# Kernel tuning notes

Measured on AMD Instinct MI355X. Metric: run time of the kernel, lower is better.

Reference implementation:

```python
import jax, jax.numpy as jnp
import numpy as np

N_EXPERTS = 32
TOPK = 256
DMODEL = 1024
EXPERT_SIZE = 2048
BATCH = 2
CUTOFF = 4096


def setup_inputs() -> dict:
    key = jax.random.key(0)
    k1, k2, k3, k4 = jax.random.split(key, 4)
    x = jax.random.normal(k1, (BATCH, CUTOFF, DMODEL), dtype=jnp.float32)
    # init scales ~ 1/sqrt(fan_in), mimicking get_init_weight
    gate = jax.random.normal(k2, (CUTOFF, N_EXPERTS), dtype=jnp.float32) / np.sqrt(DMODEL)
    lin1_weight = jax.random.normal(k3, (N_EXPERTS, DMODEL, EXPERT_SIZE), dtype=jnp.float32) / np.sqrt(DMODEL)
    lin2_weight = jax.random.normal(k4, (N_EXPERTS, EXPERT_SIZE, DMODEL), dtype=jnp.float32) / np.sqrt(EXPERT_SIZE)
    return {"x": x, "gate": gate, "lin1_weight": lin1_weight, "lin2_weight": lin2_weight}


def reference(x, gate, lin1_weight, lin2_weight):
    batch_size, cutoff, dmodel = x.shape
    n_experts = lin1_weight.shape[0]
    # gate scores: (batch, cutoff, n_experts) -> (n_experts, batch*cutoff)
    gate_out = jnp.einsum('bcd,ce->bce', x, gate)
    gate_out = jnp.transpose(gate_out, (2, 0, 1)).reshape(n_experts, batch_size * cutoff)
    probs = jax.nn.softmax(gate_out, axis=1)
    # top-k token selection per expert (computed but, faithfully to the original,
    # not used to gather tokens -- the original reshapes tokens contiguously)
    topk_values, topk_indices = jax.lax.top_k(probs, TOPK)
    # contiguous token -> expert grouping (as in the original reshape)
    xe = x.reshape(n_experts, TOPK, dmodel)  # requires batch*cutoff == n_experts*topk
    h = jax.nn.relu(jnp.einsum('ekd,eds->eks', xe, lin1_weight))
    out = jnp.einsum('eks,esd->ekd', h, lin2_weight)
    return out.reshape(batch_size, cutoff, dmodel)
```

## Files before the change

### kernel.cpp

```cpp
#include <hip/hip_runtime.h>
#include <hip/hip_bf16.h>

#define NE 32
#define MM 256
#define DM 1024
#define ES 2048

typedef __attribute__((ext_vector_type(8))) short short8;
typedef __attribute__((ext_vector_type(4))) float f32x4;
typedef unsigned int uint32;
typedef unsigned long long u64;
typedef unsigned short u16;

__device__ __forceinline__ uint32 cvt_pk_bf16(float a, float b) {
    uint32 r;
    asm("v_cvt_pk_bf16_f32 %0, %1, %2" : "=v"(r) : "v"(a), "v"(b));
    return r;
}
__device__ __forceinline__ u64 pack4(float a, float b, float c, float d) {
    return (u64)cvt_pk_bf16(a, b) | ((u64)cvt_pk_bf16(c, d) << 32);
}

__device__ __forceinline__ void gl_lds16(const void* g, void* l) {
    __builtin_amdgcn_global_load_lds(
        (const __attribute__((address_space(1))) uint32*)g,
        (__attribute__((address_space(3))) uint32*)l, 16, 0, 0);
}

__device__ __forceinline__ int b_off(int n, int k) {
    int X = ((n >> 2) & 7) ^ ((n & 3) << 1);
    return n * 128 + ((((k >> 3) ^ X) & 7) << 4) + (((k >> 2) & 1) << 3);
}

__global__ __launch_bounds__(256) void cvt_bf16(const float* __restrict__ x,
                                                u16* __restrict__ xb, int n4) {
    int i = blockIdx.x * blockDim.x + threadIdx.x;
    int stride = gridDim.x * blockDim.x;
    for (; i < n4; i += stride) {
        float4 v = ((const float4*)x)[i];
        ((u64*)xb)[i] = pack4(v.x, v.y, v.z, v.w);
    }
}

template<int N, int K, bool RELU, typename CT>
__global__ __launch_bounds__(512) void ec_gemm(
    const u16* __restrict__ A,
    const float* __restrict__ B,
    CT* __restrict__ C)
{
    constexpr int BM = 256, BN = 256, BK = 64;
    constexpr int NT = N / BN;
    constexpr int NSTEP = K / BK;
    constexpr int EPX = NE / 8;

    int bid   = blockIdx.x;
    int xcd   = bid & 7;
    int local = bid >> 3;
    int e     = xcd * EPX + local / NT;
    int nt    = local % NT;

    const u16*   Ae = A + (size_t)e * MM * K;
    const float* Be = B + (size_t)e * K * N + (size_t)nt * BN;
    CT*          Ce = C + (size_t)e * MM * N + (size_t)nt * BN;

    __shared__ char AsB[2][BM * BK * 2];
    __shared__ char BsB[2][BN * BK * 2];

    const int t    = threadIdx.x;
    const int lane = t & 63;
    const int w    = t >> 6;
    const int wm   = (w >> 2) * 128;
    const int wn   = (w & 3) * 64;
    const int lr   = lane & 15;
    const int lg   = lane >> 4;

    const int bn4 = (t & 63) * 4;
    const int bkb = (t >> 6) * 8;

    f32x4  acc[8][4] = {};
    float4 br[2][4];

    auto gloadA = [&](int kt, int buf) {
        #pragma unroll
        for (int r = 0; r < 4; ++r) {
            int reg = w * 4 + r;
            int m   = reg * 8 + (lane >> 3);
            int s   = (lane & 7) ^ (m & 7);
            const u16* g = Ae + (size_t)m * K + kt + s * 8;
            gl_lds16(g, AsB[buf] + reg * 1024);
        }
    };
    auto loadB = [&](int kt) {
        #pragma unroll
        for (int g = 0; g < 2; ++g) {
            const float* Bk = Be + (size_t)(kt + bkb + g * 4) * N + bn4;
            br[g][0] = *(const float4*)(Bk);
            br[g][1] = *(const float4*)(Bk + N);
            br[g][2] = *(const float4*)(Bk + 2 * (size_t)N);
            br[g][3] = *(const float4*)(Bk + 3 * (size_t)N);
        }
    };
    auto writeB = [&](int buf) {
        #pragma unroll
        for (int g = 0; g < 2; ++g) {
            int k4 = bkb + g * 4;
            *(u64*)(BsB[buf] + b_off(bn4 + 0, k4)) = pack4(br[g][0].x, br[g][1].x, br[g][2].x, br[g][3].x);
            *(u64*)(BsB[buf] + b_off(bn4 + 1, k4)) = pack4(br[g][0].y, br[g][1].y, br[g][2].y, br[g][3].y);
            *(u64*)(BsB[buf] + b_off(bn4 + 2, k4)) = pack4(br[g][0].z, br[g][1].z, br[g][2].z, br[g][3].z);
            *(u64*)(BsB[buf] + b_off(bn4 + 3, k4)) = pack4(br[g][0].w, br[g][1].w, br[g][2].w, br[g][3].w);
        }
    };
    auto readA = [&](int i, int k, int buf) -> short8 {
        int m = wm + i * 16 + lr;
        int s = ((k >> 3) ^ (m & 7)) & 7;
        return *(const short8*)(AsB[buf] + m * 128 + s * 16);
    };

    loadB(0);
    gloadA(0, 0);
    writeB(0);
    __syncthreads();

    for (int ks = 0; ks < NSTEP; ++ks) {
        const int  c  = ks & 1;
        const bool pf = (ks + 1 < NSTEP);
        if (pf) { gloadA((ks + 1) * BK, c ^ 1); loadB((ks + 1) * BK); }

        #pragma unroll
        for (int kk = 0; kk < 2; ++kk) {
            int k = kk * 32 + lg * 8;
            short8 af[8], bfr[4];
            #pragma unroll
            for (int i = 0; i < 8; ++i) af[i] = readA(i, k, c);
            #pragma unroll
            for (int j = 0; j < 4; ++j)
                bfr[j] = *(const short8*)(BsB[c] + b_off(wn + j * 16 + lr, k));
            #pragma unroll
            for (int i = 0; i < 8; ++i)
                #pragma unroll
                for (int j = 0; j < 4; ++j)
                    acc[i][j] = __builtin_amdgcn_mfma_f32_16x16x32_bf16(af[i], bfr[j], acc[i][j], 0, 0, 0);
        }
        if (pf) writeB(c ^ 1);
        __syncthreads();
    }

    #pragma unroll
    for (int i = 0; i < 8; ++i) {
        #pragma unroll
        for (int rr = 0; rr < 4; ++rr) {
            int row = wm + i * 16 + lg * 4 + rr;
            CT* Cp = Ce + (size_t)row * N + wn + lr;
            if constexpr (sizeof(CT) == 2) {
                #pragma unroll
                for (int jp = 0; jp < 2; ++jp) {
                    float v0 = acc[i][2 * jp + 0][rr];
                    float v1 = acc[i][2 * jp + 1][rr];
                    if constexpr (RELU) {
                        v0 = v0 > 0.0f ? v0 : 0.0f;
                        v1 = v1 > 0.0f ? v1 : 0.0f;
                    }
                    uint32 pk = cvt_pk_bf16(v0, v1);
                    ((u16*)Cp)[(2 * jp + 0) * 16] = (u16)(pk & 0xffffu);
                    ((u16*)Cp)[(2 * jp + 1) * 16] = (u16)(pk >> 16);
                }
            } else {
                #pragma unroll
                for (int j = 0; j < 4; ++j) {
                    float v = acc[i][j][rr];
                    if constexpr (RELU) v = v > 0.0f ? v : 0.0f;
                    ((float*)Cp)[j * 16] = v;
                }
            }
        }
    }
}

extern "C" void kernel_launch(void* const* d_in, const int* in_sizes, int n_in,
                              void* d_out, int out_size, void* d_ws, size_t ws_size,
                              hipStream_t stream) {
    const float* x    = (const float*)d_in[0];
    const float* lin1 = (const float*)d_in[2];
    const float* lin2 = (const float*)d_in[3];
    float* out = (float*)d_out;

    u16* h  = (u16*)d_ws;
    u16* xb = (u16*)((char*)d_ws + (size_t)36 * 1024 * 1024);

    cvt_bf16<<<2048, 256, 0, stream>>>(x, xb, NE * MM * DM / 4);
    ec_gemm<ES, DM, true,  u16  ><<<NE * (ES/256), 512, 0, stream>>>(xb, lin1, h);
    ec_gemm<DM, ES, false, float><<<NE * (DM/256), 512, 0, stream>>>(h, lin2, out);
}
```

Baseline: 185.3 us.

## Fuse both expert GEMMs into one kernel keeping hidden chunk in LDS

Replaces the two expert GEMM launches with one fused kernel. Each block computes a 256-wide chunk of the ReLU hidden activation, stores it as bf16 in shared memory, then multiplies it by the matching slice of lin2 and atomically adds partial outputs into a pre-zeroed output buffer. This removes the global round-trip of the hidden tensor and one launch, and adds nontemporal weight loads. In exchange it needs a memset, fp32 atomics from 8 chunks per output element, a single-buffered second stage with extra barriers, and 144KB of LDS, which allows only one block per CU.

New measurement: 286.5 us. 54.6% more time.

```diff
diff --git a/kernel.cpp b/kernel.cpp
--- a/kernel.cpp
+++ b/kernel.cpp
@@ -20,6 +20,11 @@
 __device__ __forceinline__ u64 pack4(float a, float b, float c, float d) {
     return (u64)cvt_pk_bf16(a, b) | ((u64)cvt_pk_bf16(c, d) << 32);
 }
+__device__ __forceinline__ u16 f2bf(float f) {
+    uint32 u = __float_as_uint(f);
+    u += 0x7fffu + ((u >> 16) & 1u);
+    return (u16)(u >> 16);
+}
 
 __device__ __forceinline__ void gl_lds16(const void* g, void* l) {
     __builtin_amdgcn_global_load_lds(
@@ -27,9 +32,16 @@
         (__attribute__((address_space(3))) uint32*)l, 16, 0, 0);
 }
 
+__device__ __forceinline__ f32x4 nt_load4(const float* p) {
+    return __builtin_nontemporal_load((const f32x4*)p);
+}
+
 __device__ __forceinline__ int b_off(int n, int k) {
     int X = ((n >> 2) & 7) ^ ((n & 3) << 1);
     return n * 128 + ((((k >> 3) ^ X) & 7) << 4) + (((k >> 2) & 1) << 3);
+}
+__device__ __forceinline__ int h_off(int m, int k) {
+    return m * 512 + (((k >> 3) ^ (m & 7)) << 4) + (k & 7) * 2;
 }
 
 __global__ __launch_bounds__(256) void cvt_bf16(const float* __restrict__ x,
@@ -37,141 +49,203 @@
     int i = blockIdx.x * blockDim.x + threadIdx.x;
     int stride = gridDim.x * blockDim.x;
     for (; i < n4; i += stride) {
-        float4 v = ((const float4*)x)[i];
-        ((u64*)xb)[i] = pack4(v.x, v.y, v.z, v.w);
+        f32x4 v = __builtin_nontemporal_load(&((const f32x4*)x)[i]);
+        ((u64*)xb)[i] = pack4(v[0], v[1], v[2], v[3]);
     }
 }
 
-template<int N, int K, bool RELU, typename CT>
-__global__ __launch_bounds__(512) void ec_gemm(
-    const u16* __restrict__ A,
-    const float* __restrict__ B,
-    CT* __restrict__ C)
+__global__ __launch_bounds__(512) void ec_fused(
+    const u16*  __restrict__ A,
+    const float* __restrict__ B1,
+    const float* __restrict__ B2,
+    float* __restrict__ C)
 {
-    constexpr int BM = 256, BN = 256, BK = 64;
-    constexpr int NT = N / BN;
-    constexpr int NSTEP = K / BK;
-    constexpr int EPX = NE / 8;
+    constexpr int BK = 64;
+    constexpr int NSTEP1 = DM / BK;
 
     int bid   = blockIdx.x;
     int xcd   = bid & 7;
     int local = bid >> 3;
-    int e     = xcd * EPX + local / NT;
-    int nt    = local % NT;
-
-    const u16*   Ae = A + (size_t)e * MM * K;
-    const float* Be = B + (size_t)e * K * N + (size_t)nt * BN;
-    CT*          Ce = C + (size_t)e * MM * N + (size_t)nt * BN;
-
-    __shared__ char AsB[2][BM * BK * 2];
-    __shared__ char BsB[2][BN * BK * 2];
+    int e     = xcd * (NE / 8) + local / 8;
+    int ch    = local % 8;
+
+    const u16*   Ae  = A  + (size_t)e * MM * DM;
+    const float* B1e = B1 + (size_t)e * DM * ES + (size_t)ch * 256;
+    const float* B2e = B2 + (size_t)e * ES * DM + (size_t)ch * 256 * DM;
+    float*       Ce  = C  + (size_t)e * MM * DM;
+
+    __shared__ char pool[144 * 1024];
+    char* HL  = pool;
+    char* B2L = pool + 128 * 1024;
 
     const int t    = threadIdx.x;
     const int lane = t & 63;
     const int w    = t >> 6;
-    const int wm   = (w >> 2) * 128;
-    const int wn   = (w & 3) * 64;
     const int lr   = lane & 15;
     const int lg   = lane >> 4;
 
-    const int bn4 = (t & 63) * 4;
-    const int bkb = (t >> 6) * 8;
-
-    f32x4  acc[8][4] = {};
-    float4 br[2][4];
-
-    auto gloadA = [&](int kt, int buf) {
+    {
+        const int wm = (w >> 2) * 128;
+        const int wn = (w & 3) * 64;
+        const int bn4 = (t & 63) * 4;
+        const int bkb = (t >> 6) * 8;
+
+        f32x4 acc[8][4] = {};
+        f32x4 br[2][4];
+
+        auto gloadA = [&](int kt, int buf) {
+            #pragma unroll
+            for (int r = 0; r < 4; ++r) {
+                int reg = w * 4 + r;
+                int m   = reg * 8 + (lane >> 3);
+                int s   = (lane & 7) ^ (m & 7);
+                gl_lds16(Ae + (size_t)m * DM + kt + s * 8,
+                         pool + buf * 32 * 1024 + reg * 1024);
+            }
+        };
+        auto loadB = [&](int kt) {
+            #pragma unroll
+            for (int g = 0; g < 2; ++g) {
+                const float* Bk = B1e + (size_t)(kt + bkb + g * 4) * ES + bn4;
+                br[g][0] = nt_load4(Bk);
+                br[g][1] = nt_load4(Bk + ES);
+                br[g][2] = nt_load4(Bk + 2 * (size_t)ES);
+                br[g][3] = nt_load4(Bk + 3 * (size_t)ES);
+            }
+        };
+        auto writeB = [&](int buf) {
+            char* bb = pool + 64 * 1024 + buf * 32 * 1024;
+            #pragma unroll
+            for (int g = 0; g < 2; ++g) {
+                int k4 = bkb + g * 4;
+                *(u64*)(bb + b_off(bn4 + 0, k4)) = pack4(br[g][0][0], br[g][1][0], br[g][2][0], br[g][3][0]);
+                *(u64*)(bb + b_off(bn4 + 1, k4)) = pack4(br[g][0][1], br[g][1][1], br[g][2][1], br[g][3][1]);
+                *(u64*)(bb + b_off(bn4 + 2, k4)) = pack4(br[g][0][2], br[g][1][2], br[g][2][2], br[g][3][2]);
+                *(u64*)(bb + b_off(bn4 + 3, k4)) = pack4(br[g][0][3], br[g][1][3], br[g][2][3], br[g][3][3]);
+            }
+        };
+
+        loadB(0);
+        gloadA(0, 0);
+        writeB(0);
+        __syncthreads();
+
+        for (int ks = 0; ks < NSTEP1; ++ks) {
+            const int  c  = ks & 1;
+            const bool pf = (ks + 1 < NSTEP1);
+            if (pf) { gloadA((ks + 1) * BK, c ^ 1); loadB((ks + 1) * BK); }
+
+            const char* ab = pool + c * 32 * 1024;
+            const char* bb = pool + 64 * 1024 + c * 32 * 1024;
+            #pragma unroll
+            for (int kk = 0; kk < 2; ++kk) {
+                int k = kk * 32 + lg * 8;
+                short8 af[8], bfr[4];
+                #pragma unroll
+                for (int i = 0; i < 8; ++i) {
+                    int m = wm + i * 16 + lr;
+                    int s = ((k >> 3) ^ (m & 7)) & 7;
+                    af[i] = *(const short8*)(ab + m * 128 + s * 16);
+                }
+                #pragma unroll
+                for (int j = 0; j < 4; ++j)
+                    bfr[j] = *(const short8*)(bb + b_off(wn + j * 16 + lr, k));
+                #pragma unroll
+                for (int i = 0; i < 8; ++i)
+                    #pragma unroll
+                    for (int j = 0; j < 4; ++j)
+                        acc[i][j] = __builtin_amdgcn_mfma_f32_16x16x32_bf16(af[i], bfr[j], acc[i][j], 0, 0, 0);
+            }
+            if (pf) writeB(c ^ 1);
+            __syncthreads();
+        }
+
         #pragma unroll
-        for (int r = 0; r < 4; ++r) {
-            int reg = w * 4 + r;
-            int m   = reg * 8 + (lane >> 3);
-            int s   = (lane & 7) ^ (m & 7);
-            const u16* g = Ae + (size_t)m * K + kt + s * 8;
-            gl_lds16(g, AsB[buf] + reg * 1024);
-        }
-    };
-    auto loadB = [&](int kt) {
-        #pragma unroll
-        for (int g = 0; g < 2; ++g) {
-            const float* Bk = Be + (size_t)(kt + bkb + g * 4) * N + bn4;
-            br[g][0] = *(const float4*)(Bk);
-            br[g][1] = *(const float4*)(Bk + N);
-            br[g][2] = *(const float4*)(Bk + 2 * (size_t)N);
-            br[g][3] = *(const float4*)(Bk + 3 * (size_t)N);
-        }
-    };
-    auto writeB = [&](int buf) {
-        #pragma unroll
-        for (int g = 0; g < 2; ++g) {
-            int k4 = bkb + g * 4;
-            *(u64*)(BsB[buf] + b_off(bn4 + 0, k4)) = pack4(br[g][0].x, br[g][1].x, br[g][2].x, br[g][3].x);
-            *(u64*)(BsB[buf] + b_off(bn4 + 1, k4)) = pack4(br[g][0].y, br[g][1].y, br[g][2].y, br[g][3].y);
-            *(u64*)(BsB[buf] + b_off(bn4 + 2, k4)) = pack4(br[g][0].z, br[g][1].z, br[g][2].z, br[g][3].z);
-            *(u64*)(BsB[buf] + b_off(bn4 + 3, k4)) = pack4(br[g][0].w, br[g][1].w, br[g][2].w, br[g][3].w);
-        }
-    };
-    auto readA = [&](int i, int k, int buf) -> short8 {
-        int m = wm + i * 16 + lr;
-        int s = ((k >> 3) ^ (m & 7)) & 7;
-        return *(const short8*)(AsB[buf] + m * 128 + s * 16);
-    };
-
-    loadB(0);
-    gloadA(0, 0);
-    writeB(0);
-    __syncthreads();
-
-    for (int ks = 0; ks < NSTEP; ++ks) {
-        const int  c  = ks & 1;
-        const bool pf = (ks + 1 < NSTEP);
-        if (pf) { gloadA((ks + 1) * BK, c ^ 1); loadB((ks + 1) * BK); }
-
-        #pragma unroll
-        for (int kk = 0; kk < 2; ++kk) {
-            int k = kk * 32 + lg * 8;
-            short8 af[8], bfr[4];
-            #pragma unroll
-            for (int i = 0; i < 8; ++i) af[i] = readA(i, k, c);
-            #pragma unroll
-            for (int j = 0; j < 4; ++j)
-                bfr[j] = *(const short8*)(BsB[c] + b_off(wn + j * 16 + lr, k));
-            #pragma unroll
-            for (int i = 0; i < 8; ++i)
-                #pragma unroll
-                for (int j = 0; j < 4; ++j)
-                    acc[i][j] = __builtin_amdgcn_mfma_f32_16x16x32_bf16(af[i], bfr[j], acc[i][j], 0, 0, 0);
-        }
-        if (pf) writeB(c ^ 1);
+        for (int i = 0; i < 8; ++i)
+            #pragma unroll
+            for (int rr = 0; rr < 4; ++rr) {
+                int row = wm + i * 16 + lg * 4 + rr;
+                #pragma unroll
+                for (int j = 0; j < 4; ++j) {
+                    float v = acc[i][j][rr];
+                    v = v > 0.0f ? v : 0.0f;
+                    int col = wn + j * 16 + lr;
+                    *(u16*)(HL + h_off(row, col)) = f2bf(v);
+                }
+            }
         __syncthreads();
     }
 
-    #pragma unroll
-    for (int i = 0; i < 8; ++i) {
-        #pragma unroll
-        for (int rr = 0; rr < 4; ++rr) {
-            int row = wm + i * 16 + lg * 4 + rr;
-            CT* Cp = Ce + (size_t)row * N + wn + lr;
-            if constexpr (sizeof(CT) == 2) {
-                #pragma unroll
-                for (int jp = 0; jp < 2; ++jp) {
-                    float v0 = acc[i][2 * jp + 0][rr];
-                    float v1 = acc[i][2 * jp + 1][rr];
-                    if constexpr (RELU) {
-                        v0 = v0 > 0.0f ? v0 : 0.0f;
-                        v1 = v1 > 0.0f ? v1 : 0.0f;
+    {
+        const int wm = (w >> 1) * 64;
+        const int wn = (w & 1) * 64;
+        const int bn4 = (t & 31) * 4;
+        const int bkb = (t >> 5) * 4;
+
+        f32x4 acc2[4][4] = {};
+        f32x4 br2[4];
+
+        auto loadB2 = [&](int nt2, int ks2) {
+            const float* Bk = B2e + (size_t)(ks2 * 64 + bkb) * DM + nt2 * 128 + bn4;
+            br2[0] = nt_load4(Bk);
+            br2[1] = nt_load4(Bk + DM);
+            br2[2] = nt_load4(Bk + 2 * (size_t)DM);
+            br2[3] = nt_load4(Bk + 3 * (size_t)DM);
+        };
+        auto writeB2 = [&]() {
+            *(u64*)(B2L + b_off(bn4 + 0, bkb)) = pack4(br2[0][0], br2[1][0], br2[2][0], br2[3][0]);
+            *(u64*)(B2L + b_off(bn4 + 1, bkb)) = pack4(br2[0][1], br2[1][1], br2[2][1], br2[3][1]);
+            *(u64*)(B2L + b_off(bn4 + 2, bkb)) = pack4(br2[0][2], br2[1][2], br2[2][2], br2[3][2]);
+            *(u64*)(B2L + b_off(bn4 + 3, bkb)) = pack4(br2[0][3], br2[1][3], br2[2][3], br2[3][3]);
+        };
+
+        loadB2(0, 0);
+        writeB2();
+        __syncthreads();
+
+        for (int s = 0; s < 32; ++s) {
+            const int nt2 = s >> 2;
+            const int ks2 = s & 3;
+            const bool pf = (s + 1 < 32);
+            if (pf) loadB2((s + 1) >> 2, (s + 1) & 3);
+
+            #pragma unroll
+            for (int kk = 0; kk < 2; ++kk) {
+                int kl = kk * 32 + lg * 8;
+                int kg = ks2 * 64 + kl;
+                short8 af[4], bfr[4];
+                #pragma unroll
+                for (int i = 0; i < 4; ++i) {
+                    int m = wm + i * 16 + lr;
+                    af[i] = *(const short8*)(HL + m * 512 + (((kg >> 3) ^ (m & 7)) << 4));
+                }
+                #pragma unroll
+                for (int j = 0; j < 4; ++j)
+                    bfr[j] = *(const short8*)(B2L + b_off(wn + j * 16 + lr, kl));
+                #pragma unroll
+                for (int i = 0; i < 4; ++i)
+                    #pragma unroll
+                    for (int j = 0; j < 4; ++j)
+                        acc2[i][j] = __builtin_amdgcn_mfma_f32_16x16x32_bf16(af[i], bfr[j], acc2[i][j], 0, 0, 0);
+            }
+
+            if (ks2 == 3) {
+                #pragma unroll
+                for (int i = 0; i < 4; ++i)
+                    #pragma unroll
+                    for (int rr = 0; rr < 4; ++rr) {
+                        int row = wm + i * 16 + lg * 4 + rr;
+                        float* Cp = Ce + (size_t)row * DM + nt2 * 128 + wn + lr;
+                        #pragma unroll
+                        for (int j = 0; j < 4; ++j) {
+                            unsafeAtomicAdd(&Cp[j * 16], acc2[i][j][rr]);
+                            acc2[i][j][rr] = 0.0f;
+                        }
                     }
-                    uint32 pk = cvt_pk_bf16(v0, v1);
-                    ((u16*)Cp)[(2 * jp + 0) * 16] = (u16)(pk & 0xffffu);
-                    ((u16*)Cp)[(2 * jp + 1) * 16] = (u16)(pk >> 16);
-                }
-            } else {
-                #pragma unroll
-                for (int j = 0; j < 4; ++j) {
-                    float v = acc[i][j][rr];
-                    if constexpr (RELU) v = v > 0.0f ? v : 0.0f;
-                    ((float*)Cp)[j * 16] = v;
-                }
-            }
+            }
+
+            __syncthreads();
+            if (pf) { writeB2(); __syncthreads(); }
         }
     }
 }
@@ -184,10 +258,9 @@
     const float* lin2 = (const float*)d_in[3];
     float* out = (float*)d_out;
 
-    u16* h  = (u16*)d_ws;
-    u16* xb = (u16*)((char*)d_ws + (size_t)36 * 1024 * 1024);
-
+    u16* xb = (u16*)d_ws;
+
+    (void)hipMemsetAsync(out, 0, (size_t)out_size * sizeof(float), stream);
     cvt_bf16<<<2048, 256, 0, stream>>>(x, xb, NE * MM * DM / 4);
-    ec_gemm<ES, DM, true,  u16  ><<<NE * (ES/256), 512, 0, stream>>>(xb, lin1, h);
-    ec_gemm<DM, ES, false, float><<<NE * (DM/256), 512, 0, stream>>>(h, lin2, out);
-}
+    ec_fused<<<NE * 8, 512, 0, stream>>>(xb, lin1, lin2, out);
+}
```
